# Optimization experiments

Measured on AMD Instinct MI355X. Metric: run time of the kernel, lower is better.

Reference implementation:

```python
import jax, jax.numpy as jnp
import numpy as np

EPS = 1e-5

def _layer_norm(x, w, b):
    mu = jnp.mean(x, axis=-1, keepdims=True)
    var = jnp.mean(jnp.square(x - mu), axis=-1, keepdims=True)
    return (x - mu) * jax.lax.rsqrt(var + EPS) * w + b

def setup_inputs() -> dict:
    key = jax.random.key(0)
    ks = jax.random.split(key, 8)
    B, S, D = 8, 2048, 1024
    image_features = jax.random.normal(ks[0], (B, S, D), dtype=jnp.float32)
    text_features = jax.random.normal(ks[1], (B, S, D), dtype=jnp.float32)
    ln_w = jnp.ones((D,), dtype=jnp.float32)
    ln_b = jnp.zeros((D,), dtype=jnp.float32)
    lim = 1.0 / np.sqrt(D)
    W_img = jax.random.uniform(ks[2], (D, D), minval=-lim, maxval=lim, dtype=jnp.float32)
    b_img = jax.random.uniform(ks[3], (D,), minval=-lim, maxval=lim, dtype=jnp.float32)
    W_txt = jax.random.uniform(ks[4], (D, D), minval=-lim, maxval=lim, dtype=jnp.float32)
    b_txt = jax.random.uniform(ks[5], (D,), minval=-lim, maxval=lim, dtype=jnp.float32)
    return {"image_features": image_features, "text_features": text_features,
            "ln_w": ln_w, "ln_b": ln_b, "W_img": W_img, "b_img": b_img,
            "W_txt": W_txt, "b_txt": b_txt}

def reference(image_features, text_features, ln_w, ln_b, W_img, b_img, W_txt, b_txt):
    D = image_features.shape[-1]
    scale = D ** (-0.5)
    image_norm = _layer_norm(image_features, ln_w, ln_b)
    text_norm = _layer_norm(text_features, ln_w, ln_b)
    # torch Linear: x @ W^T + b
    image_proj = jnp.einsum('bsd,ed->bse', image_norm, W_img) + b_img  # [B,Si,D]
    text_proj = jnp.einsum('btd,ed->bte', text_norm, W_txt) + b_txt    # [B,St,D]
    attn = jnp.einsum('bsd,btd->bst', image_proj, text_proj) * scale   # [B,Si,St]
    attn = jax.nn.softmax(attn, axis=-1)
    image_out = jnp.einsum('bst,btd->bsd', attn, text_proj)            # [B,Si,D]
    text_out = jnp.einsum('bst,bsd->btd', attn, image_proj)            # [B,St,D]
    return (image_out, text_out)
```

## Files before the change

### kernel.cpp

```cpp
#include <hip/hip_runtime.h>


#define DEV __device__ __forceinline__

typedef short s16x8 __attribute__((ext_vector_type(8)));
typedef float f32x4 __attribute__((ext_vector_type(4)));

DEV unsigned short f2bf(float f){
  unsigned u = __float_as_uint(f);
  u = (u + 0x7fffu + ((u >> 16) & 1u)) >> 16;
  return (unsigned short)u;
}
DEV float bf2f(unsigned short s){ return __uint_as_float(((unsigned)s) << 16); }

DEV void ldsload16(const void* g, void* l){
  __builtin_amdgcn_global_load_lds((const __attribute__((address_space(1))) void*)g,
                                   (__attribute__((address_space(3))) void*)l, 16, 0, 0);
}

__global__ __launch_bounds__(256) void k_cvt(const float* __restrict__ src,
                                             unsigned short* __restrict__ dst, int n4){
  int i = blockIdx.x * 256 + threadIdx.x;
  if (i < n4){
    float4 v = ((const float4*)src)[i];
    ushort4 o;
    o.x = f2bf(v.x); o.y = f2bf(v.y); o.z = f2bf(v.z); o.w = f2bf(v.w);
    ((ushort4*)dst)[i] = o;
  }
}

__global__ __launch_bounds__(256) void k_ln(const float* __restrict__ x,
                                            const float* __restrict__ w,
                                            const float* __restrict__ b,
                                            unsigned short* __restrict__ y){
  int row = blockIdx.x, tid = threadIdx.x;
  float4 v = ((const float4*)(x + (size_t)row * 1024))[tid];
  float s  = v.x + v.y + v.z + v.w;
  float s2 = v.x*v.x + v.y*v.y + v.z*v.z + v.w*v.w;
  #pragma unroll
  for (int o = 32; o > 0; o >>= 1){ s += __shfl_xor(s, o, 64); s2 += __shfl_xor(s2, o, 64); }
  __shared__ float sh[8];
  int wv = tid >> 6, ln = tid & 63;
  if (!ln){ sh[wv] = s; sh[4 + wv] = s2; }
  __syncthreads();
  s  = sh[0] + sh[1] + sh[2] + sh[3];
  s2 = sh[4] + sh[5] + sh[6] + sh[7];
  float mean = s * (1.f/1024.f);
  float var  = s2 * (1.f/1024.f) - mean * mean;
  float rstd = rsqrtf(var + 1e-5f);
  float4 w4 = ((const float4*)w)[tid];
  float4 b4 = ((const float4*)b)[tid];
  ushort4 o;
  o.x = f2bf((v.x-mean)*rstd*w4.x + b4.x);
  o.y = f2bf((v.y-mean)*rstd*w4.y + b4.y);
  o.z = f2bf((v.z-mean)*rstd*w4.z + b4.z);
  o.w = f2bf((v.w-mean)*rstd*w4.w + b4.w);
  ((ushort4*)(y + (size_t)row * 1024))[tid] = o;
}

template<int OUT_BF16>
__global__ __launch_bounds__(512, 2) void k_gemm256(const unsigned short* __restrict__ A,
                                                    const unsigned short* __restrict__ Bt,
                                                    void* __restrict__ C,
                                                    const float* __restrict__ bias, float scale,
                                                    int K, int lda, int ldb, int ldc,
                                                    long sA, long sB, long sC,
                                                    int NBX, int NBY){
  __shared__ __align__(16) unsigned short As[2][256 * 64];
  __shared__ __align__(16) unsigned short Bs[2][256 * 64];
  int nwg = gridDim.x;
  int bid = blockIdx.x;
  int swz = (bid & 7) * (nwg >> 3) + (bid >> 3);
  int bx = swz % NBX; int rem = swz / NBX;
  int by = rem % NBY; int bz = rem / NBY;

  int tid = threadIdx.x, lane = tid & 63, wave = tid >> 6;
  int wm = wave >> 2, wn = wave & 3;
  int q = lane >> 4, fr = lane & 15;
  const unsigned short* Ab = A  + (size_t)bz * sA + (size_t)by * 256 * lda;
  const unsigned short* Bb = Bt + (size_t)bz * sB + (size_t)bx * 256 * ldb;
  int sr = tid >> 3;
  int u8 = ((tid & 7) ^ (sr & 7)) * 8;
  int NT = K >> 6;

  f32x4 acc[8][4];
  #pragma unroll
  for (int m = 0; m < 8; ++m)
    #pragma unroll
    for (int n = 0; n < 4; ++n) acc[m][n] = f32x4{0.f, 0.f, 0.f, 0.f};

  #pragma unroll
  for (int i = 0; i < 4; ++i)
    ldsload16(Ab + (size_t)(i*64 + sr) * lda + u8, &As[0][(i*512 + wave*64) * 8]);
  #pragma unroll
  for (int i = 0; i < 4; ++i)
    ldsload16(Bb + (size_t)(i*64 + sr) * ldb + u8, &Bs[0][(i*512 + wave*64) * 8]);

  for (int t = 0; t < NT; ++t){
    int c = t & 1;
    asm volatile("s_waitcnt vmcnt(0)" ::: "memory");
    __builtin_amdgcn_s_barrier();
    if (t + 1 < NT){
      int ko = (t + 1) << 6;
      #pragma unroll
      for (int i = 0; i < 4; ++i)
        ldsload16(Ab + (size_t)(i*64 + sr) * lda + ko + u8, &As[c^1][(i*512 + wave*64) * 8]);
      #pragma unroll
      for (int i = 0; i < 4; ++i)
        ldsload16(Bb + (size_t)(i*64 + sr) * ldb + ko + u8, &Bs[c^1][(i*512 + wave*64) * 8]);
    }
    const unsigned short* Ap = As[c];
    const unsigned short* Bp = Bs[c];
    s16x8 bfrag[4][2];
    #pragma unroll
    for (int n = 0; n < 4; ++n){
      int r = wn*64 + n*16 + fr;
      #pragma unroll
      for (int kk = 0; kk < 2; ++kk){
        int p = (kk*4 + q) ^ (r & 7);
        bfrag[n][kk] = *(const s16x8*)&Bp[r*64 + p*8];
      }
    }
    #pragma unroll
    for (int ph = 0; ph < 4; ++ph){
      s16x8 af[2][2];
      #pragma unroll
      for (int mm = 0; mm < 2; ++mm){
        int r = wm*128 + (ph*2 + mm)*16 + fr;
        #pragma unroll
        for (int kk = 0; kk < 2; ++kk){
          int p = (kk*4 + q) ^ (r & 7);
          af[mm][kk] = *(const s16x8*)&Ap[r*64 + p*8];
        }
      }
      __builtin_amdgcn_s_barrier();
      asm volatile("s_waitcnt lgkmcnt(0)" ::: "memory");
      __builtin_amdgcn_s_setprio(1);
      #pragma unroll
      for (int mm = 0; mm < 2; ++mm)
        #pragma unroll
        for (int n = 0; n < 4; ++n)
          #pragma unroll
          for (int kk = 0; kk < 2; ++kk)
            acc[ph*2 + mm][n] = __builtin_amdgcn_mfma_f32_16x16x32_bf16(
                af[mm][kk], bfrag[n][kk], acc[ph*2 + mm][n], 0, 0, 0);
      __builtin_amdgcn_s_setprio(0);
      __builtin_amdgcn_s_barrier();
    }
  }
  size_t cb = (size_t)bz * sC;
  int row0 = by*256 + wm*128 + q*4;
  int col0 = bx*256 + wn*64 + fr;
  #pragma unroll
  for (int m = 0; m < 8; ++m){
    #pragma unroll
    for (int n = 0; n < 4; ++n){
      int col = col0 + n*16;
      float bv = bias ? bias[col] : 0.f;
      #pragma unroll
      for (int j = 0; j < 4; ++j){
        int row = row0 + m*16 + j;
        float vv = acc[m][n][j] * scale + bv;
        if (OUT_BF16) ((unsigned short*)C)[cb + (size_t)row*ldc + col] = f2bf(vv);
        else          ((float*)C)[cb + (size_t)row*ldc + col] = vv;
      }
    }
  }
}

__global__ __launch_bounds__(256) void k_transpose(const unsigned short* __restrict__ src,
                                                   unsigned short* __restrict__ dst,
                                                   int R, int C, long sS, long sD){
  __shared__ __align__(16) unsigned short tile[64 * 64];
  int tid = threadIdx.x;
  const unsigned short* sb = src + (size_t)blockIdx.z * sS;
  unsigned short* db = dst + (size_t)blockIdx.z * sD;
  int r0 = blockIdx.y * 64, c0 = blockIdx.x * 64;
  #pragma unroll
  for (int i = 0; i < 2; ++i){
    int ci = i * 256 + tid;
    int row = ci >> 3, cch = ci & 7;
    int pos = cch ^ (row & 7) ^ (row >> 3);
    uint4 v = *(const uint4*)&sb[(size_t)(r0 + row) * C + c0 + cch * 8];
    *(uint4*)&tile[row * 64 + pos * 8] = v;
  }
  __syncthreads();
  int ocp = tid >> 3, og = tid & 7;
  int oc = ocp * 2;
  union { uint4 v; unsigned short us[8]; } o0, o1;
  #pragma unroll
  for (int k = 0; k < 8; ++k){
    int r = og * 8 + k;
    int pos = (oc >> 3) ^ (r & 7) ^ (r >> 3);
    unsigned pr = *(const unsigned*)&tile[r * 64 + pos * 8 + (oc & 7)];
    o0.us[k] = (unsigned short)(pr & 0xffffu);
    o1.us[k] = (unsigned short)(pr >> 16);
  }
  *(uint4*)&db[(size_t)(c0 + oc    ) * R + r0 + og * 8] = o0.v;
  *(uint4*)&db[(size_t)(c0 + oc + 1) * R + r0 + og * 8] = o1.v;
}

__global__ __launch_bounds__(256) void k_softmax(unsigned short* __restrict__ a){
  size_t row = blockIdx.x;
  unsigned short* p = a + row * 2048;
  int tid = threadIdx.x;
  union { uint4 v; unsigned short us[8]; } in, out;
  in.v = *(const uint4*)&p[tid * 8];
  float x[8];
  #pragma unroll
  for (int j = 0; j < 8; ++j) x[j] = bf2f(in.us[j]);
  float mx = x[0];
  #pragma unroll
  for (int j = 1; j < 8; ++j) mx = fmaxf(mx, x[j]);
  #pragma unroll
  for (int o = 32; o > 0; o >>= 1) mx = fmaxf(mx, __shfl_xor(mx, o, 64));
  __shared__ float sh[8];
  int wv = tid >> 6, ln = tid & 63;
  if (!ln) sh[wv] = mx;
  __syncthreads();
  mx = fmaxf(fmaxf(sh[0], sh[1]), fmaxf(sh[2], sh[3]));
  float sm = 0.f, e[8];
  #pragma unroll
  for (int j = 0; j < 8; ++j){ e[j] = __expf(x[j] - mx); sm += e[j]; }
  #pragma unroll
  for (int o = 32; o > 0; o >>= 1) sm += __shfl_xor(sm, o, 64);
  if (!ln) sh[4 + wv] = sm;
  __syncthreads();
  sm = sh[4] + sh[5] + sh[6] + sh[7];
  float inv = 1.f / sm;
  #pragma unroll
  for (int j = 0; j < 8; ++j) out.us[j] = f2bf(e[j] * inv);
  *(uint4*)&p[tid * 8] = out.v;
}

extern "C" void kernel_launch(void* const* d_in, const int* in_sizes, int n_in,
                              void* d_out, int out_size, void* d_ws, size_t ws_size,
                              hipStream_t stream) {
  const float* img  = (const float*)d_in[0];
  const float* txt  = (const float*)d_in[1];
  const float* lnw  = (const float*)d_in[2];
  const float* lnb  = (const float*)d_in[3];
  const float* Wimg = (const float*)d_in[4];
  const float* bimg = (const float*)d_in[5];
  const float* Wtxt = (const float*)d_in[6];
  const float* btxt = (const float*)d_in[7];
  float* out = (float*)d_out;

  char* ws = (char*)d_ws;
  unsigned short* R1 = (unsigned short*)ws;
  unsigned short* R2 = (unsigned short*)(ws + 67108864);
  unsigned short* WB = (unsigned short*)(ws + 134217728);
  unsigned short* R4 = (unsigned short*)(ws + 138412032);

  const long PB = 2097152;
  const long AB = 4194304;

  k_cvt<<<1024, 256, 0, stream>>>(Wimg, WB,           262144);
  k_cvt<<<1024, 256, 0, stream>>>(Wtxt, WB + 1048576, 262144);
  k_ln<<<16384, 256, 0, stream>>>(img, lnw, lnb, R1);
  k_ln<<<16384, 256, 0, stream>>>(txt, lnw, lnb, R1 + 16777216);
  k_gemm256<1><<<256, 512, 0, stream>>>(R1,            WB,           R2,            bimg, 1.f,
                                        1024, 1024, 1024, 1024, 0, 0, 0, 4, 64);
  k_gemm256<1><<<256, 512, 0, stream>>>(R1 + 16777216, WB + 1048576, R2 + 16777216, btxt, 1.f,
                                        1024, 1024, 1024, 1024, 0, 0, 0, 4, 64);
  dim3 gt(16, 32, 8);
  k_transpose<<<gt, 256, 0, stream>>>(R2,            R1,            2048, 1024, PB, PB);
  k_transpose<<<gt, 256, 0, stream>>>(R2 + 16777216, R1 + 16777216, 2048, 1024, PB, PB);
  k_gemm256<1><<<512, 512, 0, stream>>>(R2, R2 + 16777216, R4, nullptr, 0.03125f,
                                        1024, 1024, 1024, 2048, PB, PB, AB, 8, 8);
  k_softmax<<<16384, 256, 0, stream>>>(R4);
  dim3 gat(32, 32, 8);
  k_transpose<<<gat, 256, 0, stream>>>(R4, R2, 2048, 2048, AB, AB);
  k_gemm256<0><<<256, 512, 0, stream>>>(R4, R1 + 16777216, out, nullptr, 1.f,
                                        2048, 2048, 2048, 1024, AB, PB, PB, 4, 8);
  k_gemm256<0><<<256, 512, 0, stream>>>(R2, R1, out + 16777216, nullptr, 1.f,
                                        2048, 2048, 2048, 1024, AB, PB, PB, 4, 8);
}
```

Before: 461.5 us.

## Restructure GEMM mainloop into 8-phase pipeline with split half-K LDS stages

Splits each 64-wide K tile into two 32-wide halves stored in separate LDS buffers with a new XOR swizzle. The main loop now processes two K tiles per iteration over 8 phases, interleaving the global-to-LDS loads of future halves with MFMA work. It uses partial vmcnt waits instead of draining all loads each tile. The aim is to hide global load latency behind compute and shorten barrier stalls, at the cost of more complex wait/barrier bookkeeping and an assumption that K is a multiple of 128.

New measurement: 439.7 us. 1.05x faster.

```diff
diff --git a/kernel.cpp b/kernel.cpp
--- a/kernel.cpp
+++ b/kernel.cpp
@@ -58,6 +58,13 @@
   ((ushort4*)(y + (size_t)row * 1024))[tid] = o;
 }
 
+#define STG(MAT, BASE, LD, T, H) do{                                              \
+  ldsload16((BASE) + (size_t)(rl      ) * (LD) + (T)*64 + (H)*32 + g8,            \
+            &MAT[(T)&1][H][(wave*16)*32]);                                        \
+  ldsload16((BASE) + (size_t)(rl + 128) * (LD) + (T)*64 + (H)*32 + g8,            \
+            &MAT[(T)&1][H][(128 + wave*16)*32]);                                  \
+}while(0)
+
 template<int OUT_BF16>
 __global__ __launch_bounds__(512, 2) void k_gemm256(const unsigned short* __restrict__ A,
                                                     const unsigned short* __restrict__ Bt,
@@ -66,8 +73,8 @@
                                                     int K, int lda, int ldb, int ldc,
                                                     long sA, long sB, long sC,
                                                     int NBX, int NBY){
-  __shared__ __align__(16) unsigned short As[2][256 * 64];
-  __shared__ __align__(16) unsigned short Bs[2][256 * 64];
+  __shared__ __align__(16) unsigned short As[2][2][8192];
+  __shared__ __align__(16) unsigned short Bs[2][2][8192];
   int nwg = gridDim.x;
   int bid = blockIdx.x;
   int swz = (bid & 7) * (nwg >> 3) + (bid >> 3);
@@ -79,9 +86,12 @@
   int q = lane >> 4, fr = lane & 15;
   const unsigned short* Ab = A  + (size_t)bz * sA + (size_t)by * 256 * lda;
   const unsigned short* Bb = Bt + (size_t)bz * sB + (size_t)bx * 256 * ldb;
-  int sr = tid >> 3;
-  int u8 = ((tid & 7) ^ (sr & 7)) * 8;
-  int NT = K >> 6;
+  int rl = wave*16 + (lane>>2);
+  int g8 = (((lane&3) ^ ((lane>>2)&3) ^ ((lane>>4)&3))) * 8;
+  int qp8 = ((q ^ (lane&3) ^ ((lane>>2)&3))) * 8;
+  int aro = (wm*128 + fr)*32 + qp8;
+  int bro = (wn*64  + fr)*32 + qp8;
+  int NT = K >> 6, niter = K >> 7;
 
   f32x4 acc[8][4];
   #pragma unroll
@@ -89,63 +99,56 @@
     #pragma unroll
     for (int n = 0; n < 4; ++n) acc[m][n] = f32x4{0.f, 0.f, 0.f, 0.f};
 
-  #pragma unroll
-  for (int i = 0; i < 4; ++i)
-    ldsload16(Ab + (size_t)(i*64 + sr) * lda + u8, &As[0][(i*512 + wave*64) * 8]);
-  #pragma unroll
-  for (int i = 0; i < 4; ++i)
-    ldsload16(Bb + (size_t)(i*64 + sr) * ldb + u8, &Bs[0][(i*512 + wave*64) * 8]);
-
-  for (int t = 0; t < NT; ++t){
-    int c = t & 1;
-    asm volatile("s_waitcnt vmcnt(0)" ::: "memory");
-    __builtin_amdgcn_s_barrier();
-    if (t + 1 < NT){
-      int ko = (t + 1) << 6;
-      #pragma unroll
-      for (int i = 0; i < 4; ++i)
-        ldsload16(Ab + (size_t)(i*64 + sr) * lda + ko + u8, &As[c^1][(i*512 + wave*64) * 8]);
-      #pragma unroll
-      for (int i = 0; i < 4; ++i)
-        ldsload16(Bb + (size_t)(i*64 + sr) * ldb + ko + u8, &Bs[c^1][(i*512 + wave*64) * 8]);
-    }
-    const unsigned short* Ap = As[c];
-    const unsigned short* Bp = Bs[c];
-    s16x8 bfrag[4][2];
+  STG(Bs, Bb, ldb, 0, 0);
+  STG(As, Ab, lda, 0, 0);
+  STG(Bs, Bb, ldb, 0, 1);
+  STG(As, Ab, lda, 0, 1);
+  asm volatile("s_waitcnt vmcnt(4)" ::: "memory");
+  asm volatile("s_barrier" ::: "memory");
+
+  for (int i = 0; i < niter; ++i){
+    s16x8 bf[4];
     #pragma unroll
-    for (int n = 0; n < 4; ++n){
-      int r = wn*64 + n*16 + fr;
-      #pragma unroll
-      for (int kk = 0; kk < 2; ++kk){
-        int p = (kk*4 + q) ^ (r & 7);
-        bfrag[n][kk] = *(const s16x8*)&Bp[r*64 + p*8];
-      }
-    }
-    #pragma unroll
-    for (int ph = 0; ph < 4; ++ph){
-      s16x8 af[2][2];
-      #pragma unroll
-      for (int mm = 0; mm < 2; ++mm){
-        int r = wm*128 + (ph*2 + mm)*16 + fr;
-        #pragma unroll
-        for (int kk = 0; kk < 2; ++kk){
-          int p = (kk*4 + q) ^ (r & 7);
-          af[mm][kk] = *(const s16x8*)&Ap[r*64 + p*8];
+    for (int ph = 0; ph < 8; ++ph){
+      const int buf = ph >> 2;
+      const int kk  = (ph >> 1) & 1;
+      const unsigned short* Ah = &As[buf][kk][0];
+      const unsigned short* Bh = &Bs[buf][kk][0];
+      s16x8 af[4];
+      if ((ph & 1) == 0){
+        #pragma unroll
+        for (int n = 0; n < 4; ++n) bf[n] = *(const s16x8*)&Bh[bro + n*512];
+        #pragma unroll
+        for (int mi = 0; mi < 4; ++mi) af[mi] = *(const s16x8*)&Ah[aro + mi*512];
+      } else {
+        #pragma unroll
+        for (int mi = 0; mi < 4; ++mi) af[mi] = *(const s16x8*)&Ah[aro + (4+mi)*512];
+      }
+      {
+        int tgt = 2*i + ((ph < 4) ? 1 : 2);
+        if (tgt < NT){
+          const int h = (ph >> 1) & 1;
+          if (ph & 1) STG(As, Ab, lda, tgt, h);
+          else        STG(Bs, Bb, ldb, tgt, h);
         }
       }
-      __builtin_amdgcn_s_barrier();
+      asm volatile("s_barrier" ::: "memory");
       asm volatile("s_waitcnt lgkmcnt(0)" ::: "memory");
       __builtin_amdgcn_s_setprio(1);
       #pragma unroll
-      for (int mm = 0; mm < 2; ++mm)
+      for (int mi = 0; mi < 4; ++mi)
         #pragma unroll
         for (int n = 0; n < 4; ++n)
-          #pragma unroll
-          for (int kk = 0; kk < 2; ++kk)
-            acc[ph*2 + mm][n] = __builtin_amdgcn_mfma_f32_16x16x32_bf16(
-                af[mm][kk], bfrag[n][kk], acc[ph*2 + mm][n], 0, 0, 0);
+          acc[(ph&1)*4 + mi][n] = __builtin_amdgcn_mfma_f32_16x16x32_bf16(
+              af[mi], bf[n], acc[(ph&1)*4 + mi][n], 0, 0, 0);
       __builtin_amdgcn_s_setprio(0);
-      __builtin_amdgcn_s_barrier();
+      if (ph & 1){
+        if (i + 1 < niter || ph < 5)
+          asm volatile("s_waitcnt vmcnt(4)" ::: "memory");
+        else if (ph == 5)
+          asm volatile("s_waitcnt vmcnt(0)" ::: "memory");
+      }
+      asm volatile("s_barrier" ::: "memory");
     }
   }
   size_t cb = (size_t)bz * sC;
```
